# Optimization experiments

Measured on AMD Instinct MI355X. Metric: run time of the kernel, lower is better.

Reference implementation:

```python
import jax, jax.numpy as jnp
import numpy as np

T_STEPS = 30
HIDDEN = 16
INPUT_DIM = 32
OUTPUT_DIM = 1
BATCH = 262144


def setup_inputs() -> dict:
    key = jax.random.key(0)
    ks = jax.random.split(key, 8)
    u = lambda k, shape: jax.random.uniform(k, shape, jnp.float32, -0.25, 0.25)
    return {
        "x": jax.random.normal(ks[0], (BATCH, INPUT_DIM), jnp.float32),
        "T": T_STEPS,
        "W_ih": u(ks[1], (HIDDEN, INPUT_DIM)),
        "W_hh": u(ks[2], (HIDDEN, HIDDEN)),
        "b_ih": u(ks[3], (HIDDEN,)),
        "b_hh": u(ks[4], (HIDDEN,)),
        "W_fc": jax.random.normal(ks[5], (OUTPUT_DIM, HIDDEN), jnp.float32) * 0.25,
        "b_fc": jax.random.normal(ks[6], (OUTPUT_DIM,), jnp.float32) * 0.25,
    }


def reference(x, T, W_ih, W_hh, b_ih, b_hh, W_fc, b_fc):
    # Input is the same at every timestep (x repeated T times), so the
    # input projection is computed once and reused across the scan.
    xproj = x @ W_ih.T + b_ih + b_hh  # [B, H]
    h0 = jnp.zeros((x.shape[0], W_hh.shape[0]), dtype=x.dtype)

    def step(h, _):
        h = jnp.tanh(xproj + h @ W_hh.T)  # Elman: tanh(Wx+b_ih + Uh+b_hh)
        return h, h

    _, hs = jax.lax.scan(step, h0, None, length=T)  # [T, B, H]
    hs = jnp.transpose(hs, (1, 0, 2))               # [B, T, H] (batch_first)
    return hs @ W_fc.T + b_fc                       # [B, T, output_dim]
```

## Files before the change

### kernel.cpp

```cpp
#include <hip/hip_runtime.h>


#define T_STEPS 30
#define BLOCK   256
#define SCALE   2.8853900817779268f

typedef _Float16 v4h __attribute__((ext_vector_type(4)));
typedef __fp16   v2fp __attribute__((ext_vector_type(2)));
typedef float    v4f __attribute__((ext_vector_type(4)));

struct h4 { v2fp lo, hi; };

__global__ __launch_bounds__(BLOCK, 8) void rnn_mfma(
    const float* __restrict__ x,
    const float* __restrict__ W_ih,
    const float* __restrict__ W_hh,
    const float* __restrict__ b_ih,
    const float* __restrict__ b_hh,
    const float* __restrict__ W_fc,
    const float* __restrict__ b_fc,
    float* __restrict__ out)
{
    __shared__ float tmp[64 * T_STEPS];

    const int tid  = threadIdx.x;
    const int w    = tid >> 6;
    const int lane = tid & 63;
    const int r    = lane & 15;
    const int q    = lane >> 4;
    const int j0   = 4 * q;

    const size_t row = (size_t)blockIdx.x * 64 + (size_t)w * 16 + r;

    float a0 = b_ih[j0 + 0] + b_hh[j0 + 0];
    float a1 = b_ih[j0 + 1] + b_hh[j0 + 1];
    float a2 = b_ih[j0 + 2] + b_hh[j0 + 2];
    float a3 = b_ih[j0 + 3] + b_hh[j0 + 3];
    {
        const float4* xrow = (const float4*)(x + row * 32);
#pragma unroll
        for (int c4 = 0; c4 < 8; ++c4) {
            float4 xv = xrow[c4];
            const float4 w0 = *(const float4*)(W_ih + (j0 + 0) * 32 + c4 * 4);
            const float4 w1 = *(const float4*)(W_ih + (j0 + 1) * 32 + c4 * 4);
            const float4 w2 = *(const float4*)(W_ih + (j0 + 2) * 32 + c4 * 4);
            const float4 w3 = *(const float4*)(W_ih + (j0 + 3) * 32 + c4 * 4);
            a0 = fmaf(w0.x, xv.x, fmaf(w0.y, xv.y, fmaf(w0.z, xv.z, fmaf(w0.w, xv.w, a0))));
            a1 = fmaf(w1.x, xv.x, fmaf(w1.y, xv.y, fmaf(w1.z, xv.z, fmaf(w1.w, xv.w, a1))));
            a2 = fmaf(w2.x, xv.x, fmaf(w2.y, xv.y, fmaf(w2.z, xv.z, fmaf(w2.w, xv.w, a2))));
            a3 = fmaf(w3.x, xv.x, fmaf(w3.y, xv.y, fmaf(w3.z, xv.z, fmaf(w3.w, xv.w, a3))));
        }
    }
    const v4f xpv = {a0 * SCALE, a1 * SCALE, a2 * SCALE, a3 * SCALE};

    v4h whh;
    {
        float4 wr = *(const float4*)(W_hh + r * 16 + 4 * q);
        whh[0] = (_Float16)(wr.x * SCALE);
        whh[1] = (_Float16)(wr.y * SCALE);
        whh[2] = (_Float16)(wr.z * SCALE);
        whh[3] = (_Float16)(wr.w * SCALE);
    }

    v4h afc;
#pragma unroll
    for (int i = 0; i < 4; ++i) {
        float wv = W_fc[4 * q + i];
        _Float16 hi = (_Float16)wv;
        _Float16 lo = (_Float16)(wv - (float)hi);
        afc[i] = (r == 0) ? hi : ((r == 1) ? lo : (_Float16)0.0f);
    }
    const float bfc = b_fc[0];
    const v4f zfc = {(q == 0) ? bfc : 0.0f, 0.0f, 0.0f, 0.0f};

    v4h s = {(_Float16)0.0f, (_Float16)0.0f, (_Float16)0.0f, (_Float16)0.0f};

    float* myout = &tmp[(w * 16 + r) * T_STEPS];

#pragma unroll
    for (int t = 0; t < T_STEPS; ++t) {
        v4f acc = __builtin_amdgcn_mfma_f32_16x16x16f16(whh, s, xpv, 0, 0, 0);

        float e0 = __builtin_amdgcn_exp2f(acc[0]);
        float e1 = __builtin_amdgcn_exp2f(acc[1]);
        float e2 = __builtin_amdgcn_exp2f(acc[2]);
        float e3 = __builtin_amdgcn_exp2f(acc[3]);
        float d0 = 1.0f + e0;
        float d1 = 1.0f + e1;
        float d2 = 1.0f + e2;
        float d3 = 1.0f + e3;
        float m01 = d0 * d1;
        float m23 = d2 * d3;
        float rr  = __builtin_amdgcn_rcpf(m01 * m23);
        float r01 = rr * m23;
        float r23 = rr * m01;
        float h0 = fmaf(-2.0f, r01 * d1, 1.0f);
        float h1 = fmaf(-2.0f, r01 * d0, 1.0f);
        float h2 = fmaf(-2.0f, r23 * d3, 1.0f);
        float h3 = fmaf(-2.0f, r23 * d2, 1.0f);

        h4 p;
        p.lo = __builtin_amdgcn_cvt_pkrtz(h0, h1);
        p.hi = __builtin_amdgcn_cvt_pkrtz(h2, h3);
        s = __builtin_bit_cast(v4h, p);

        v4f f = __builtin_amdgcn_mfma_f32_16x16x16f16(afc, s, zfc, 0, 0, 0);

        if (lane < 16)
            myout[t] = f[0] + f[1];
    }

    __syncthreads();

    float* oblk = out + (size_t)blockIdx.x * (64 * T_STEPS);
    for (int idx = tid; idx < 64 * T_STEPS; idx += BLOCK)
        oblk[idx] = tmp[idx];
}

extern "C" void kernel_launch(void* const* d_in, const int* in_sizes, int n_in,
                              void* d_out, int out_size, void* d_ws, size_t ws_size,
                              hipStream_t stream) {
    const float* x    = (const float*)d_in[0];
    const float* W_ih = (const float*)d_in[2];
    const float* W_hh = (const float*)d_in[3];
    const float* b_ih = (const float*)d_in[4];
    const float* b_hh = (const float*)d_in[5];
    const float* W_fc = (const float*)d_in[6];
    const float* b_fc = (const float*)d_in[7];
    float* out = (float*)d_out;

    const int B = in_sizes[0] / 32;
    const int grid = B / 64;

    rnn_mfma<<<grid, BLOCK, 0, stream>>>(x, W_ih, W_hh, b_ih, b_hh, W_fc, b_fc, out);
}
```

Before: 129.4 us.

## Compute input projection with split-fp16 MFMA and defer output stores in pairs

Replaces the per-lane scalar FMA input projection (each lane reading a full 32-float x row plus 16 W_ih rows) with six MFMA 16x16x16 ops. They use hi/lo fp16 splits of x and the scaled W_ih to keep near-fp32 accuracy, and the bias is folded into the accumulator. The per-step output MFMA results are now buffered across two timesteps and written as float2 LDS stores, one step late, so the store no longer waits on the latest MFMA result. This cuts redundant global loads and VALU work in the prologue, at the cost of extra conversion instructions and slightly different rounding.

New measurement: 116.1 us. 10.3% less time.

```diff
diff --git a/kernel.cpp b/kernel.cpp
--- a/kernel.cpp
+++ b/kernel.cpp
@@ -10,6 +10,13 @@
 typedef float    v4f __attribute__((ext_vector_type(4)));
 
 struct h4 { v2fp lo, hi; };
+
+static __device__ __forceinline__ v4h pack4(float a, float b, float c, float d) {
+    h4 p;
+    p.lo = __builtin_amdgcn_cvt_pkrtz(a, b);
+    p.hi = __builtin_amdgcn_cvt_pkrtz(c, d);
+    return __builtin_bit_cast(v4h, p);
+}
 
 __global__ __launch_bounds__(BLOCK, 8) void rnn_mfma(
     const float* __restrict__ x,
@@ -32,26 +39,40 @@
 
     const size_t row = (size_t)blockIdx.x * 64 + (size_t)w * 16 + r;
 
-    float a0 = b_ih[j0 + 0] + b_hh[j0 + 0];
-    float a1 = b_ih[j0 + 1] + b_hh[j0 + 1];
-    float a2 = b_ih[j0 + 2] + b_hh[j0 + 2];
-    float a3 = b_ih[j0 + 3] + b_hh[j0 + 3];
+    v4f xpv;
     {
-        const float4* xrow = (const float4*)(x + row * 32);
-#pragma unroll
-        for (int c4 = 0; c4 < 8; ++c4) {
-            float4 xv = xrow[c4];
-            const float4 w0 = *(const float4*)(W_ih + (j0 + 0) * 32 + c4 * 4);
-            const float4 w1 = *(const float4*)(W_ih + (j0 + 1) * 32 + c4 * 4);
-            const float4 w2 = *(const float4*)(W_ih + (j0 + 2) * 32 + c4 * 4);
-            const float4 w3 = *(const float4*)(W_ih + (j0 + 3) * 32 + c4 * 4);
-            a0 = fmaf(w0.x, xv.x, fmaf(w0.y, xv.y, fmaf(w0.z, xv.z, fmaf(w0.w, xv.w, a0))));
-            a1 = fmaf(w1.x, xv.x, fmaf(w1.y, xv.y, fmaf(w1.z, xv.z, fmaf(w1.w, xv.w, a1))));
-            a2 = fmaf(w2.x, xv.x, fmaf(w2.y, xv.y, fmaf(w2.z, xv.z, fmaf(w2.w, xv.w, a2))));
-            a3 = fmaf(w3.x, xv.x, fmaf(w3.y, xv.y, fmaf(w3.z, xv.z, fmaf(w3.w, xv.w, a3))));
-        }
+        const float4 x0 = *(const float4*)(x + row * 32 + 4 * q);
+        const float4 x1 = *(const float4*)(x + row * 32 + 16 + 4 * q);
+        float4 w0 = *(const float4*)(W_ih + r * 32 + 4 * q);
+        float4 w1 = *(const float4*)(W_ih + r * 32 + 16 + 4 * q);
+        w0.x *= SCALE; w0.y *= SCALE; w0.z *= SCALE; w0.w *= SCALE;
+        w1.x *= SCALE; w1.y *= SCALE; w1.z *= SCALE; w1.w *= SCALE;
+
+        v4h xh0 = pack4(x0.x, x0.y, x0.z, x0.w);
+        v4h xh1 = pack4(x1.x, x1.y, x1.z, x1.w);
+        v4h wh0 = pack4(w0.x, w0.y, w0.z, w0.w);
+        v4h wh1 = pack4(w1.x, w1.y, w1.z, w1.w);
+        v4h xl0 = pack4(x0.x - (float)xh0[0], x0.y - (float)xh0[1],
+                        x0.z - (float)xh0[2], x0.w - (float)xh0[3]);
+        v4h xl1 = pack4(x1.x - (float)xh1[0], x1.y - (float)xh1[1],
+                        x1.z - (float)xh1[2], x1.w - (float)xh1[3]);
+        v4h wl0 = pack4(w0.x - (float)wh0[0], w0.y - (float)wh0[1],
+                        w0.z - (float)wh0[2], w0.w - (float)wh0[3]);
+        v4h wl1 = pack4(w1.x - (float)wh1[0], w1.y - (float)wh1[1],
+                        w1.z - (float)wh1[2], w1.w - (float)wh1[3]);
+
+        const float4 bi = *(const float4*)(b_ih + j0);
+        const float4 bh = *(const float4*)(b_hh + j0);
+        v4f c = {SCALE * (bi.x + bh.x), SCALE * (bi.y + bh.y),
+                 SCALE * (bi.z + bh.z), SCALE * (bi.w + bh.w)};
+
+        xpv = __builtin_amdgcn_mfma_f32_16x16x16f16(wh0, xh0, c,   0, 0, 0);
+        xpv = __builtin_amdgcn_mfma_f32_16x16x16f16(wh1, xh1, xpv, 0, 0, 0);
+        xpv = __builtin_amdgcn_mfma_f32_16x16x16f16(wh0, xl0, xpv, 0, 0, 0);
+        xpv = __builtin_amdgcn_mfma_f32_16x16x16f16(wh1, xl1, xpv, 0, 0, 0);
+        xpv = __builtin_amdgcn_mfma_f32_16x16x16f16(wl0, xh0, xpv, 0, 0, 0);
+        xpv = __builtin_amdgcn_mfma_f32_16x16x16f16(wl1, xh1, xpv, 0, 0, 0);
     }
-    const v4f xpv = {a0 * SCALE, a1 * SCALE, a2 * SCALE, a3 * SCALE};
 
     v4h whh;
     {
@@ -77,6 +98,8 @@
 
     float* myout = &tmp[(w * 16 + r) * T_STEPS];
 
+    v4f fe, fo;
+
 #pragma unroll
     for (int t = 0; t < T_STEPS; ++t) {
         v4f acc = __builtin_amdgcn_mfma_f32_16x16x16f16(whh, s, xpv, 0, 0, 0);
@@ -99,15 +122,25 @@
         float h2 = fmaf(-2.0f, r23 * d3, 1.0f);
         float h3 = fmaf(-2.0f, r23 * d2, 1.0f);
 
-        h4 p;
-        p.lo = __builtin_amdgcn_cvt_pkrtz(h0, h1);
-        p.hi = __builtin_amdgcn_cvt_pkrtz(h2, h3);
-        s = __builtin_bit_cast(v4h, p);
+        s = pack4(h0, h1, h2, h3);
 
-        v4f f = __builtin_amdgcn_mfma_f32_16x16x16f16(afc, s, zfc, 0, 0, 0);
-
-        if (lane < 16)
-            myout[t] = f[0] + f[1];
+        if ((t & 1) == 0) {
+            if (t >= 2 && lane < 16) {
+                float2 g;
+                g.x = fe[0] + fe[1];
+                g.y = fo[0] + fo[1];
+                *(float2*)(myout + (t - 2)) = g;
+            }
+            fe = __builtin_amdgcn_mfma_f32_16x16x16f16(afc, s, zfc, 0, 0, 0);
+        } else {
+            fo = __builtin_amdgcn_mfma_f32_16x16x16f16(afc, s, zfc, 0, 0, 0);
+        }
+    }
+    if (lane < 16) {
+        float2 g;
+        g.x = fe[0] + fe[1];
+        g.y = fo[0] + fo[1];
+        *(float2*)(myout + (T_STEPS - 2)) = g;
     }
 
     __syncthreads();
```
